# Kernel optimization log

Hardware: AMD Instinct MI355X
Metric: run time of the kernel (lower is better)

Reference implementation:

```python
import jax, jax.numpy as jnp
import numpy as np

# ---- constants from FlyingCartpole.__init__ defaults ----
MASS_Q = 2.0
MASS_P = 0.1
MASS = MASS_Q + MASS_P              # total mass m
JMAT = jnp.array([[0.0023, 0.0, 0.0], [0.0, 0.0023, 0.0], [0.0, 0.0, 0.004]], jnp.float32)
JINV = jnp.linalg.inv(JMAT)
L = 0.5                              # pendulum length
GVEC = jnp.array([0.0, 0.0, -9.81], jnp.float32)
MOTOR_DIST = 0.175
KF = 1.0
KM = 0.025
DT = 0.05
ACT_SCALE = 10.0
U_HOVER = -MASS * (-9.81) / ACT_SCALE / KF / 4.0   # per-motor hover throttle
_SS = np.array([[1.0, 1, 0], [1.0, -1, 0], [-1.0, -1, 0], [-1.0, 1, 0]], np.float32)
SS = jnp.asarray(_SS / np.linalg.norm(_SS, axis=-1, keepdims=True))  # [4,3] unit arms


def mrp2quat(m):
    # q = [1 - |m|^2, 2m] / (1 + |m|^2)
    n2 = jnp.sum(m * m, axis=-1, keepdims=True)
    return jnp.concatenate([1.0 - n2, 2.0 * m], axis=-1) / (1.0 + n2)


def quatrot(q, v):
    # rotate vector v by unit quaternion q = [s, qv]
    s, qv = q[..., :1], q[..., 1:]
    return v + 2.0 * jnp.cross(qv, jnp.cross(qv, v) + s * v)


def w2pdotkinematics_mrp(m, w):
    # mdot = 1/4 [(1-|m|^2) I + 2 [m]_x + 2 m m^T] w
    n2 = jnp.sum(m * m, axis=-1, keepdims=True)
    mw = jnp.sum(m * w, axis=-1, keepdims=True)
    return 0.25 * ((1.0 - n2) * w + 2.0 * jnp.cross(m, w) + 2.0 * m * mw)


def dynamics_(x, u):
    # state: [r(3), m(3), theta(1), v(3), w(3), theta_dot(1)]
    u = ACT_SCALE * (u + U_HOVER)
    m = x[..., 3:6]
    v = x[..., 7:10]
    w = x[..., 10:13]
    theta = x[..., 6:7]
    theta_dot = x[..., 13:14]

    q = mrp2quat(m)

    # forces (body frame): thrust + gravity rotated by q(-m)
    Fz = KF * jnp.sum(u, axis=-1)                     # [B]
    z = jnp.zeros_like(Fz)
    Fvec = jnp.stack([z, z, Fz], axis=-1)             # [B,3]
    f = Fvec + quatrot(mrp2quat(-m), MASS * GVEC)     # [B,3]

    # moments
    tau3 = KM * (u[..., 0] - u[..., 1] + u[..., 2] - u[..., 3])
    tau = jnp.stack([z, z, tau3], axis=-1)            # [B,3]
    zu = jnp.zeros_like(u)
    thrust = jnp.stack([zu, zu, KF * u], axis=-1)     # [B,4,3]
    tau = tau + jnp.cross(MOTOR_DIST * SS, thrust).sum(axis=-2)

    mdot = w2pdotkinematics_mrp(m, w)
    pdot = quatrot(q, v)
    vdot = f / MASS - jnp.cross(w, v)
    Jw = jnp.einsum('ij,bj->bi', JMAT, w)
    wdot = jnp.einsum('ij,bj->bi', JINV, tau - jnp.cross(w, Jw))

    x_ddot = quatrot(q, vdot)[..., 0:1]
    theta_ddot = (GVEC[2] * jnp.sin(theta) + x_ddot * jnp.cos(theta)) / L
    return jnp.concatenate([pdot, mdot, theta_dot, vdot, wdot, theta_ddot], axis=-1)


def rk4_dynamics(x, u):
    dt, dt2 = DT, DT / 2.0
    k1 = dynamics_(x, u)
    k2 = dynamics_(x + dt2 * k1, u)
    k3 = dynamics_(x + dt2 * k2, u)
    k4 = dynamics_(x + dt * k3, u)
    return x + dt / 6.0 * (k1 + 2.0 * k2 + 2.0 * k3 + k4)


def setup_inputs() -> dict:
    key = jax.random.key(0)
    kx, ku = jax.random.split(key)
    B = 2097152
    x = jax.random.normal(kx, (B, 14), dtype=jnp.float32)
    u = jax.random.normal(ku, (B, 4), dtype=jnp.float32)
    return {"x": x, "u": u}


def reference(x, u):
    return rk4_dynamics(x, u)
```

## Files before the change

### kernel.cpp

```cpp
#include <hip/hip_runtime.h>
#include <math.h>

namespace fc {

typedef float vf2 __attribute__((ext_vector_type(2)));
typedef float vf4 __attribute__((ext_vector_type(4)));

__device__ __forceinline__ vf2 sp(float c) { return vf2{c, c}; }

constexpr float ACT_SCALE = 10.0f;
constexpr float U_HOVER   = 0.515025f;
constexpr float INV_MASS  = 1.0f / 2.1f;
constexpr float KM        = 0.025f;
constexpr float TAUC      = 0.175f * 0.70710678f;
constexpr float JXY       = 0.0023f;
constexpr float JZ        = 0.004f;
constexpr float INV_JXY   = 1.0f / 0.0023f;
constexpr float INV_JZ    = 1.0f / 0.004f;
constexpr float G3        = -9.81f;
constexpr float INV_L     = 2.0f;
constexpr float DT        = 0.05f;
constexpr float DT2       = 0.05f * 0.5f;
constexpr float DT6       = 0.05f / 6.0f;

__device__ __forceinline__ void dyn2(const vf2* xt, vf2 FzM,
                                     vf2 taux, vf2 tauy, vf2 tauz, vf2* dx) {
  vf2 mx = xt[3], my = xt[4], mz = xt[5], th = xt[6];
  vf2 vx = xt[7], vy = xt[8], vz = xt[9];
  vf2 wx = xt[10], wy = xt[11], wz = xt[12];

  vf2 n2 = mx * mx + my * my + mz * mz;
  vf2 inv;
  inv.x = __builtin_amdgcn_rcpf(1.0f + n2.x);
  inv.y = __builtin_amdgcn_rcpf(1.0f + n2.y);
  vf2 s  = (sp(1.0f) - n2) * inv;
  vf2 qx = sp(2.0f) * mx * inv;
  vf2 qy = sp(2.0f) * my * inv;
  vf2 qz = sp(2.0f) * mz * inv;

  vf2 gtx = qy * sp(-G3);
  vf2 gty = qx * sp(G3);
  vf2 gtz = s * sp(G3);
  vf2 gx = sp(-2.0f) * (qy * gtz - qz * gty);
  vf2 gy = sp(-2.0f) * (qz * gtx - qx * gtz);
  vf2 gz = sp(G3) + sp(-2.0f) * (qx * gty - qy * gtx);

  vf2 tx = qy * vz - qz * vy + s * vx;
  vf2 ty = qz * vx - qx * vz + s * vy;
  vf2 tz = qx * vy - qy * vx + s * vz;
  dx[0] = vx + sp(2.0f) * (qy * tz - qz * ty);
  dx[1] = vy + sp(2.0f) * (qz * tx - qx * tz);
  dx[2] = vz + sp(2.0f) * (qx * ty - qy * tx);

  vf2 mw  = mx * wx + my * wy + mz * wz;
  vf2 on2 = sp(1.0f) - n2;
  dx[3] = sp(0.25f) * (on2 * wx + sp(2.0f) * (my * wz - mz * wy) + sp(2.0f) * mx * mw);
  dx[4] = sp(0.25f) * (on2 * wy + sp(2.0f) * (mz * wx - mx * wz) + sp(2.0f) * my * mw);
  dx[5] = sp(0.25f) * (on2 * wz + sp(2.0f) * (mx * wy - my * wx) + sp(2.0f) * mz * mw);

  dx[6] = xt[13];

  vf2 vdx = gx - (wy * vz - wz * vy);
  vf2 vdy = gy - (wz * vx - wx * vz);
  vf2 vdz = FzM + gz - (wx * vy - wy * vx);
  dx[7] = vdx; dx[8] = vdy; dx[9] = vdz;

  vf2 Jwx = sp(JXY) * wx, Jwy = sp(JXY) * wy, Jwz = sp(JZ) * wz;
  dx[10] = (taux - (wy * Jwz - wz * Jwy)) * sp(INV_JXY);
  dx[11] = (tauy - (wz * Jwx - wx * Jwz)) * sp(INV_JXY);
  dx[12] = (tauz - (wx * Jwy - wy * Jwx)) * sp(INV_JZ);

  vf2 t2y = qz * vdx - qx * vdz + s * vdy;
  vf2 t2z = qx * vdy - qy * vdx + s * vdz;
  vf2 rx  = vdx + sp(2.0f) * (qy * t2z - qz * t2y);
  vf2 st, ct;
  st.x = __sinf(th.x); st.y = __sinf(th.y);
  ct.x = __cosf(th.x); ct.y = __cosf(th.y);
  dx[13] = (sp(G3) * st + rx * ct) * sp(INV_L);
}

__device__ __forceinline__ void rk4_core(const vf2* x0, vf2 FzM,
                                         vf2 taux, vf2 tauy, vf2 tauz, vf2* o) {
  vf2 xt[14], kk[14], acc[14];
  dyn2(x0, FzM, taux, tauy, tauz, kk);
  #pragma unroll
  for (int j = 0; j < 14; ++j) { acc[j] = kk[j]; xt[j] = x0[j] + sp(DT2) * kk[j]; }
  dyn2(xt, FzM, taux, tauy, tauz, kk);
  #pragma unroll
  for (int j = 0; j < 14; ++j) { acc[j] += sp(2.0f) * kk[j]; xt[j] = x0[j] + sp(DT2) * kk[j]; }
  dyn2(xt, FzM, taux, tauy, tauz, kk);
  #pragma unroll
  for (int j = 0; j < 14; ++j) { acc[j] += sp(2.0f) * kk[j]; xt[j] = x0[j] + sp(DT) * kk[j]; }
  dyn2(xt, FzM, taux, tauy, tauz, kk);
  #pragma unroll
  for (int j = 0; j < 14; ++j) o[j] = x0[j] + sp(DT6) * (acc[j] + kk[j]);
}

__device__ __forceinline__ void utau(vf4 uA, vf4 uB, vf2& FzM,
                                     vf2& taux, vf2& tauy, vf2& tauz) {
  vf2 su0 = sp(ACT_SCALE) * (vf2{uA.x, uB.x} + sp(U_HOVER));
  vf2 su1 = sp(ACT_SCALE) * (vf2{uA.y, uB.y} + sp(U_HOVER));
  vf2 su2 = sp(ACT_SCALE) * (vf2{uA.z, uB.z} + sp(U_HOVER));
  vf2 su3 = sp(ACT_SCALE) * (vf2{uA.w, uB.w} + sp(U_HOVER));
  vf2 Fz  = ((su0 + su1) + su2) + su3;
  FzM  = Fz * sp(INV_MASS);
  tauz = sp(KM) * (((su0 - su1) + su2) - su3);
  taux = ((sp(TAUC) * su0 + sp(-TAUC) * su1) + sp(-TAUC) * su2) + sp(TAUC) * su3;
  tauy = ((sp(-TAUC) * su0 + sp(-TAUC) * su1) + sp(TAUC) * su2) + sp(TAUC) * su3;
}

__global__ __launch_bounds__(128) void fc_rk4_kernel(const float* __restrict__ x,
                                                     const float* __restrict__ u,
                                                     float* __restrict__ out,
                                                     int n) {
  __shared__ float xs[2 * 1792];
  const int t = threadIdx.x;
  const int lane = t & 63;
  const int w = t >> 6;
  const long long base = (long long)blockIdx.x * 256;

  if (base + 256 <= (long long)n) {
    const long long wrow = base + w * 128;
    float* ws = xs + w * 1792;

    typedef const __attribute__((address_space(1))) float gbl_f;
    gbl_f* gsrc = (gbl_f*)(x + wrow * 14);
    #pragma unroll
    for (int k = 0; k < 7; ++k)
      __builtin_amdgcn_global_load_lds(
          (const __attribute__((address_space(1))) void*)(gsrc + k * 256 + lane * 4),
          (__attribute__((address_space(3))) void*)((__attribute__((address_space(3))) float*)ws + k * 256),
          16, 0, 0);

    const vf4* ug = (const vf4*)(u + wrow * 4);
    vf4 uA = ug[2 * lane], uB = ug[2 * lane + 1];
    vf2 FzM, taux, tauy, tauz;
    utau(uA, uB, FzM, taux, tauy, tauz);

    asm volatile("s_waitcnt vmcnt(0)" ::: "memory");

    vf4* mine = (vf4*)(ws + lane * 28);
    vf4 a0 = mine[0], a1 = mine[1], a2 = mine[2], a3 = mine[3],
        a4 = mine[4], a5 = mine[5], a6 = mine[6];
    vf2 x0[14] = {
      {a0.x, a3.z}, {a0.y, a3.w}, {a0.z, a4.x}, {a0.w, a4.y},
      {a1.x, a4.z}, {a1.y, a4.w}, {a1.z, a5.x}, {a1.w, a5.y},
      {a2.x, a5.z}, {a2.y, a5.w}, {a2.z, a6.x}, {a2.w, a6.y},
      {a3.x, a6.z}, {a3.y, a6.w}};

    vf2 o[14];
    rk4_core(x0, FzM, taux, tauy, tauz, o);

    mine[0] = vf4{o[0].x,  o[1].x,  o[2].x,  o[3].x};
    mine[1] = vf4{o[4].x,  o[5].x,  o[6].x,  o[7].x};
    mine[2] = vf4{o[8].x,  o[9].x,  o[10].x, o[11].x};
    mine[3] = vf4{o[12].x, o[13].x, o[0].y,  o[1].y};
    mine[4] = vf4{o[2].y,  o[3].y,  o[4].y,  o[5].y};
    mine[5] = vf4{o[6].y,  o[7].y,  o[8].y,  o[9].y};
    mine[6] = vf4{o[10].y, o[11].y, o[12].y, o[13].y};
    asm volatile("s_waitcnt lgkmcnt(0)" ::: "memory");

    const vf4* ws4 = (const vf4*)ws;
    vf4* og4 = (vf4*)(out + wrow * 14);
    #pragma unroll
    for (int k = 0; k < 7; ++k)
      __builtin_nontemporal_store(ws4[k * 64 + lane], og4 + k * 64 + lane);
  } else {
    #pragma unroll
    for (int k = 0; k < 2; ++k) {
      long long r = base + 2LL * t + k;
      if (r < n) {
        vf2 x0[14];
        #pragma unroll
        for (int j = 0; j < 14; ++j) { float v = x[r * 14 + j]; x0[j] = vf2{v, v}; }
        vf4 uv = *(const vf4*)(u + r * 4);
        vf2 FzM, taux, tauy, tauz;
        utau(uv, uv, FzM, taux, tauy, tauz);
        vf2 o[14];
        rk4_core(x0, FzM, taux, tauy, tauz, o);
        #pragma unroll
        for (int j = 0; j < 14; ++j) out[r * 14 + j] = o[j].x;
      }
    }
  }
}

}

extern "C" void kernel_launch(void* const* d_in, const int* in_sizes, int n_in,
                              void* d_out, int out_size, void* d_ws, size_t ws_size,
                              hipStream_t stream) {
  const float* x = (const float*)d_in[0];
  const float* u = (const float*)d_in[1];
  float* out = (float*)d_out;
  const int n = in_sizes[0] / 14;
  const int grid = (n + 255) / 256;
  hipLaunchKernelGGL(fc::fc_rk4_kernel, dim3(grid), dim3(128), 0, stream,
                     x, u, out, n);
}
```

Before: 45.65 us.

## Process two row tiles per wave with software-pipelined LDS staging

Each wave now handles two 128-row tiles, issuing both tiles' async global-to-LDS loads up front. It computes the first tile while the second is still in flight, using partial vmcnt waits. The aim is to overlap memory latency with compute and halve the grid size. In exchange, LDS use per block doubles, which may lower occupancy, and the fixed vmcnt counts depend on the exact order the compiler issues loads.

```diff
diff --git a/kernel.cpp b/kernel.cpp
--- a/kernel.cpp
+++ b/kernel.cpp
@@ -113,35 +113,44 @@
                                                      const float* __restrict__ u,
                                                      float* __restrict__ out,
                                                      int n) {
-  __shared__ float xs[2 * 1792];
+  __shared__ float xs[2 * 2 * 1792];
   const int t = threadIdx.x;
   const int lane = t & 63;
   const int w = t >> 6;
-  const long long base = (long long)blockIdx.x * 256;
-
-  if (base + 256 <= (long long)n) {
-    const long long wrow = base + w * 128;
-    float* ws = xs + w * 1792;
+  const long long base = (long long)blockIdx.x * 512;
+
+  if (base + 512 <= (long long)n) {
+    const long long r0 = base + w * 256;
+    const long long r1 = r0 + 128;
+    float* ws0 = xs + w * 3584;
+    float* ws1 = ws0 + 1792;
 
     typedef const __attribute__((address_space(1))) float gbl_f;
-    gbl_f* gsrc = (gbl_f*)(x + wrow * 14);
-    #pragma unroll
-    for (int k = 0; k < 7; ++k)
-      __builtin_amdgcn_global_load_lds(
-          (const __attribute__((address_space(1))) void*)(gsrc + k * 256 + lane * 4),
-          (__attribute__((address_space(3))) void*)((__attribute__((address_space(3))) float*)ws + k * 256),
-          16, 0, 0);
-
-    const vf4* ug = (const vf4*)(u + wrow * 4);
-    vf4 uA = ug[2 * lane], uB = ug[2 * lane + 1];
-    vf2 FzM, taux, tauy, tauz;
-    utau(uA, uB, FzM, taux, tauy, tauz);
-
-    asm volatile("s_waitcnt vmcnt(0)" ::: "memory");
-
-    vf4* mine = (vf4*)(ws + lane * 28);
-    vf4 a0 = mine[0], a1 = mine[1], a2 = mine[2], a3 = mine[3],
-        a4 = mine[4], a5 = mine[5], a6 = mine[6];
+    auto stage = [&](long long row, float* dst) {
+      gbl_f* gsrc = (gbl_f*)(x + row * 14);
+      #pragma unroll
+      for (int k = 0; k < 7; ++k)
+        __builtin_amdgcn_global_load_lds(
+            (const __attribute__((address_space(1))) void*)(gsrc + k * 256 + lane * 4),
+            (__attribute__((address_space(3))) void*)((__attribute__((address_space(3))) float*)dst + k * 256),
+            16, 0, 0);
+    };
+
+    stage(r0, ws0);
+    const vf4* ug0 = (const vf4*)(u + r0 * 4);
+    vf4 uA0 = ug0[2 * lane], uB0 = ug0[2 * lane + 1];
+    stage(r1, ws1);
+    const vf4* ug1 = (const vf4*)(u + r1 * 4);
+    vf4 uA1 = ug1[2 * lane], uB1 = ug1[2 * lane + 1];
+
+    vf2 FzM0, tx0, ty0, tz0;
+    utau(uA0, uB0, FzM0, tx0, ty0, tz0);
+
+    asm volatile("s_waitcnt vmcnt(9)" ::: "memory");
+
+    vf4* mine0 = (vf4*)(ws0 + lane * 28);
+    vf4 a0 = mine0[0], a1 = mine0[1], a2 = mine0[2], a3 = mine0[3],
+        a4 = mine0[4], a5 = mine0[5], a6 = mine0[6];
     vf2 x0[14] = {
       {a0.x, a3.z}, {a0.y, a3.w}, {a0.z, a4.x}, {a0.w, a4.y},
       {a1.x, a4.z}, {a1.y, a4.w}, {a1.z, a5.x}, {a1.w, a5.y},
@@ -149,26 +158,58 @@
       {a3.x, a6.z}, {a3.y, a6.w}};
 
     vf2 o[14];
-    rk4_core(x0, FzM, taux, tauy, tauz, o);
-
-    mine[0] = vf4{o[0].x,  o[1].x,  o[2].x,  o[3].x};
-    mine[1] = vf4{o[4].x,  o[5].x,  o[6].x,  o[7].x};
-    mine[2] = vf4{o[8].x,  o[9].x,  o[10].x, o[11].x};
-    mine[3] = vf4{o[12].x, o[13].x, o[0].y,  o[1].y};
-    mine[4] = vf4{o[2].y,  o[3].y,  o[4].y,  o[5].y};
-    mine[5] = vf4{o[6].y,  o[7].y,  o[8].y,  o[9].y};
-    mine[6] = vf4{o[10].y, o[11].y, o[12].y, o[13].y};
+    rk4_core(x0, FzM0, tx0, ty0, tz0, o);
+
+    mine0[0] = vf4{o[0].x,  o[1].x,  o[2].x,  o[3].x};
+    mine0[1] = vf4{o[4].x,  o[5].x,  o[6].x,  o[7].x};
+    mine0[2] = vf4{o[8].x,  o[9].x,  o[10].x, o[11].x};
+    mine0[3] = vf4{o[12].x, o[13].x, o[0].y,  o[1].y};
+    mine0[4] = vf4{o[2].y,  o[3].y,  o[4].y,  o[5].y};
+    mine0[5] = vf4{o[6].y,  o[7].y,  o[8].y,  o[9].y};
+    mine0[6] = vf4{o[10].y, o[11].y, o[12].y, o[13].y};
     asm volatile("s_waitcnt lgkmcnt(0)" ::: "memory");
 
-    const vf4* ws4 = (const vf4*)ws;
-    vf4* og4 = (vf4*)(out + wrow * 14);
+    const vf4* ws04 = (const vf4*)ws0;
+    vf4* og0 = (vf4*)(out + r0 * 14);
     #pragma unroll
     for (int k = 0; k < 7; ++k)
-      __builtin_nontemporal_store(ws4[k * 64 + lane], og4 + k * 64 + lane);
+      __builtin_nontemporal_store(ws04[k * 64 + lane], og0 + k * 64 + lane);
+
+    vf2 FzM1, tx1, ty1, tz1;
+    utau(uA1, uB1, FzM1, tx1, ty1, tz1);
+
+    asm volatile("s_waitcnt vmcnt(7)" ::: "memory");
+
+    vf4* mine1 = (vf4*)(ws1 + lane * 28);
+    vf4 b0 = mine1[0], b1 = mine1[1], b2 = mine1[2], b3 = mine1[3],
+        b4 = mine1[4], b5 = mine1[5], b6 = mine1[6];
+    vf2 x1[14] = {
+      {b0.x, b3.z}, {b0.y, b3.w}, {b0.z, b4.x}, {b0.w, b4.y},
+      {b1.x, b4.z}, {b1.y, b4.w}, {b1.z, b5.x}, {b1.w, b5.y},
+      {b2.x, b5.z}, {b2.y, b5.w}, {b2.z, b6.x}, {b2.w, b6.y},
+      {b3.x, b6.z}, {b3.y, b6.w}};
+
+    vf2 o1[14];
+    rk4_core(x1, FzM1, tx1, ty1, tz1, o1);
+
+    mine1[0] = vf4{o1[0].x,  o1[1].x,  o1[2].x,  o1[3].x};
+    mine1[1] = vf4{o1[4].x,  o1[5].x,  o1[6].x,  o1[7].x};
+    mine1[2] = vf4{o1[8].x,  o1[9].x,  o1[10].x, o1[11].x};
+    mine1[3] = vf4{o1[12].x, o1[13].x, o1[0].y,  o1[1].y};
+    mine1[4] = vf4{o1[2].y,  o1[3].y,  o1[4].y,  o1[5].y};
+    mine1[5] = vf4{o1[6].y,  o1[7].y,  o1[8].y,  o1[9].y};
+    mine1[6] = vf4{o1[10].y, o1[11].y, o1[12].y, o1[13].y};
+    asm volatile("s_waitcnt lgkmcnt(0)" ::: "memory");
+
+    const vf4* ws14 = (const vf4*)ws1;
+    vf4* og1 = (vf4*)(out + r1 * 14);
+    #pragma unroll
+    for (int k = 0; k < 7; ++k)
+      __builtin_nontemporal_store(ws14[k * 64 + lane], og1 + k * 64 + lane);
   } else {
     #pragma unroll
-    for (int k = 0; k < 2; ++k) {
-      long long r = base + 2LL * t + k;
+    for (int k = 0; k < 4; ++k) {
+      long long r = base + t + 128LL * k;
       if (r < n) {
         vf2 x0[14];
         #pragma unroll
@@ -194,7 +235,7 @@
   const float* u = (const float*)d_in[1];
   float* out = (float*)d_out;
   const int n = in_sizes[0] / 14;
-  const int grid = (n + 255) / 256;
+  const int grid = (n + 511) / 512;
   hipLaunchKernelGGL(fc::fc_rk4_kernel, dim3(grid), dim3(128), 0, stream,
                      x, u, out, n);
 }
```

After: 46.29 us. No clear change (+1.4%).
